# Optimization experiments

Hardware: AMD Instinct MI355X
Metric: run time of the kernel (lower is better)

The kernel has to match this reference:

```python
import jax, jax.numpy as jnp
import numpy as np

LOCAL_SIZE = 128
LN_EPS = 1e-5


def _ln(x):
    # F.layer_norm over last axis, no affine params
    mu = jnp.mean(x, axis=-1, keepdims=True)
    var = jnp.var(x, axis=-1, keepdims=True)
    return (x - mu) / jnp.sqrt(var + LN_EPS)


def _rel_shift(x):
    # x: [b, n, qlen, klen] -> Transformer-XL relative shift
    b, n, q, k = x.shape
    xp = jnp.pad(x, ((0, 0), (0, 0), (0, 0), (1, 0)))
    xp = xp.reshape(b, n, k + 1, q)
    return xp[:, :, 1:, :].reshape(b, n, q, k)


def setup_inputs() -> dict:
    key = jax.random.key(0)
    ks = jax.random.split(key, 12)
    bsz, d_model, qlen, mlen = 16, 1024, 256, 256
    n_head, d_head, d_inner = 16, 64, 4096
    klen = qlen + mlen
    s = 0.02  # param init scale
    return {
        "z1ss": jax.random.normal(ks[0], (bsz, d_model, qlen), jnp.float32),
        "uss": jax.random.normal(ks[1], (bsz, 3 * n_head * d_head, klen), jnp.float32) * 0.1,
        "mems": jax.random.normal(ks[2], (bsz, d_model, mlen), jnp.float32),
        "pos_emb": jax.random.normal(ks[3], (d_model, klen), jnp.float32),
        "Wqkv": jax.random.normal(ks[4], (3 * n_head * d_head, d_model), jnp.float32) * s,
        "Wr": jax.random.normal(ks[5], (n_head * d_head, d_model), jnp.float32) * s,
        "Wo": jax.random.normal(ks[6], (d_model, n_head * d_head), jnp.float32) * s,
        "bo": jnp.zeros((d_model,), jnp.float32),
        "r_w_bias": jax.random.uniform(ks[7], (n_head, d_head), jnp.float32, -0.05, 0.05),
        "r_r_bias": jax.random.uniform(ks[8], (n_head, d_head), jnp.float32, -0.05, 0.05),
        "W1": jax.random.normal(ks[9], (d_inner, d_model), jnp.float32) * s,
        "b1": jnp.zeros((d_inner,), jnp.float32),
        "W2": jax.random.normal(ks[10], (d_model, d_inner), jnp.float32) * s,
        "b2": jnp.zeros((d_model,), jnp.float32),
    }


def reference(z1ss, uss, mems, pos_emb, Wqkv, Wr, Wo, bo, r_w_bias, r_r_bias, W1, b1, W2, b2):
    bsz, d_model, qlen = z1ss.shape
    mlen = mems.shape[-1]
    n_head, d_head = r_w_bias.shape
    scale = 1.0 / (d_head ** 0.5)

    # ---- self-attention with relative positions ----
    cat = jnp.concatenate([mems, z1ss], axis=-1)            # [b, d, klen]
    klen = cat.shape[-1]
    w_heads = jnp.einsum('od,bdk->bok', Wqkv, cat) + uss     # [b, 3*n*dh, klen]
    r_head_k = (Wr @ pos_emb).reshape(n_head, d_head, -1)    # [n, dh, rlen]

    q, k, v = jnp.split(w_heads, 3, axis=1)
    q = q[:, :, -qlen:].reshape(bsz, n_head, d_head, qlen)   # [b, n, dh, q]
    k = k.reshape(bsz, n_head, d_head, klen)
    v = v.reshape(bsz, n_head, d_head, klen)

    AC = jnp.einsum('bndi,bndj->bnij', q + r_w_bias[:, :, None], k)
    BD = jnp.einsum('bndi,ndj->bnij', q + r_r_bias[:, :, None], r_head_k)
    BD = _rel_shift(BD)
    attn_score = (AC + BD) * scale                            # [b, n, q, klen]

    # causal + local-window mask
    i = jnp.arange(qlen)[:, None]
    j = jnp.arange(klen)[None, :]
    mask = (j > i + mlen) | (j <= i + mlen - LOCAL_SIZE)      # [q, klen]
    attn_score = jnp.where(mask[None, None], -1e30, attn_score)

    attn_prob = jax.nn.softmax(attn_score, axis=-1)
    attn_vec = jnp.einsum('bnij,bndj->bndi', attn_prob, v)    # [b, n, dh, q]
    attn_vec = attn_vec.reshape(bsz, n_head * d_head, qlen)
    attn_out = jnp.einsum('od,bdq->boq', Wo, attn_vec) + bo[None, :, None]

    # post-LN residual (pre_lnorm=False), work in [b, q, d]
    h = _ln((attn_out + z1ss).transpose(0, 2, 1))             # [b, q, d]

    # ---- position-wise FF ----
    ff = jax.nn.relu(jnp.einsum('bqd,id->bqi', h, W1) + b1)
    ff = jnp.einsum('bqi,di->bqd', ff, W2) + b2
    out = _ln(ff + h)                                          # [b, q, d]
    return out.transpose(0, 2, 1)                              # [b, d, q]
```

## Files before the change

kernel.cpp:

```cpp
#include <hip/hip_runtime.h>
#include <hip/hip_bf16.h>
#include <math.h>

#define BSZ    16
#define DMODEL 1024
#define QLEN   256
#define MLEN   256
#define KLEN   512
#define NHEAD  16
#define DHEAD  64
#define DINNER 4096

typedef __bf16 bf16;
typedef bf16 bf16x8 __attribute__((ext_vector_type(8)));
typedef float f32x4 __attribute__((ext_vector_type(4)));

#define GLOBAL_AS __attribute__((address_space(1)))
#define LDS_AS    __attribute__((address_space(3)))

__global__ __launch_bounds__(256) void prep_k(
    const float* __restrict__ Wqkv, const float* __restrict__ Wr,
    const float* __restrict__ Wo,   const float* __restrict__ W1,
    const float* __restrict__ W2,   const float* __restrict__ uss,
    const float* __restrict__ mems, const float* __restrict__ z1ss,
    const float* __restrict__ pos_emb,
    bf16* __restrict__ WqkvB, bf16* __restrict__ WrB, bf16* __restrict__ WoB,
    bf16* __restrict__ W1B,   bf16* __restrict__ W2B, bf16* __restrict__ ussV,
    bf16* __restrict__ catT,  bf16* __restrict__ posT,
    bf16* __restrict__ ussQ,  bf16* __restrict__ ussK)
{
    if (blockIdx.x < 21504) {
        long long i = (long long)blockIdx.x * 256 + threadIdx.x;
        const float* src; bf16* dst; long long soff, doff;
        if      (i <  786432) { src = Wqkv; dst = WqkvB; soff = doff = i; }
        else if (i < 1048576) { src = Wr;   dst = WrB;   soff = doff = i -  786432; }
        else if (i < 1310720) { src = Wo;   dst = WoB;   soff = doff = i - 1048576; }
        else if (i < 2359296) { src = W1;   dst = W1B;   soff = doff = i - 1310720; }
        else if (i < 3407872) { src = W2;   dst = W2B;   soff = doff = i - 2359296; }
        else {
            long long u = i - 3407872, b = u >> 17, r = u & 131071;
            src = uss; dst = ussV; soff = b * 393216 + 262144 + r; doff = u;
        }
        float4 v = ((const float4*)src)[soff];
        bf16 b0 = (bf16)v.x, b1 = (bf16)v.y, b2 = (bf16)v.z, b3 = (bf16)v.w;
        union { ushort u[4]; uint2 d; } p;
        p.u[0] = *(ushort*)&b0; p.u[1] = *(ushort*)&b1;
        p.u[2] = *(ushort*)&b2; p.u[3] = *(ushort*)&b3;
        ((uint2*)dst)[doff] = p.d;
        return;
    }
    __shared__ float tile[32][33];
    int blk = blockIdx.x - 21504;
    const float* src; bf16* dst; long long soff, dof; int ld, ldo, tr, tc;
    if (blk < 8192) {
        int bh = blk >> 8, t = blk & 255;
        int b = bh >> 1, half = bh & 1;
        tr = t >> 3; tc = t & 7;
        src = half ? z1ss : mems; soff = (long long)b * 1024 * 256; ld = 256;
        dst = catT; dof = ((long long)b * 512 + half * 256) * 1024; ldo = 1024;
    } else if (blk < 8704) {
        int u = blk - 8192; tr = u >> 4; tc = u & 15;
        src = pos_emb; soff = 0; ld = 512;
        dst = posT; dof = 0; ldo = 1024;
    } else if (blk < 12800) {
        int u = blk - 8704; int b = u >> 8, t = u & 255;
        tr = t >> 3; tc = t & 7;
        src = uss; soff = (long long)b * 3072 * 512 + 256; ld = 512;
        dst = ussQ; dof = (long long)b * 256 * 1024; ldo = 1024;
    } else {
        int u = blk - 12800; int b = u >> 9, t = u & 511;
        tr = t >> 4; tc = t & 15;
        src = uss; soff = ((long long)b * 3072 + 1024) * 512; ld = 512;
        dst = ussK; dof = (long long)b * 512 * 1024; ldo = 1024;
    }
    int tx = threadIdx.x & 31, ty = threadIdx.x >> 5;
    const float* ip = src + soff;
#pragma unroll
    for (int yy = ty; yy < 32; yy += 8)
        tile[yy][tx] = ip[(long long)(tr * 32 + yy) * ld + tc * 32 + tx];
    __syncthreads();
#pragma unroll
    for (int yy = ty; yy < 32; yy += 8)
        dst[dof + (long long)(tc * 32 + yy) * ldo + tr * 32 + tx] = (bf16)tile[tx][yy];
}

__global__ __launch_bounds__(256) void qkv_gemm_k(
    const bf16* __restrict__ catT, const bf16* __restrict__ WqkvB,
    const bf16* __restrict__ posT, const bf16* __restrict__ WrB,
    const bf16* __restrict__ ussQ, const bf16* __restrict__ ussK,
    const bf16* __restrict__ ussV,
    bf16* __restrict__ qT, bf16* __restrict__ kT,
    bf16* __restrict__ rhkT, bf16* __restrict__ vB)
{
    __shared__ bf16 lA[2 * 128 * 32];
    __shared__ bf16 lB[2 * 128 * 32];

    int f = blockIdx.x;
    int id = (f & 7) * 164 + (f >> 3);
    int t = threadIdx.x;
    int w = t >> 6, lane = t & 63;

    const bf16 *Ap, *Bp;
    int mode, bz = 0, m0, n0;
    if (id < 768) {
        bz = id / 48; int r = id % 48;
        if (r < 32) { m0 = 256 + ((r >> 4) << 7); n0 = (r & 15) << 7; }
        else        { int rr = r - 32; m0 = (rr >> 3) << 7; n0 = (8 + (rr & 7)) << 7; }
        Ap = catT + (long long)bz * 512 * 1024; Bp = WqkvB; mode = 0;
    } else if (id < 800) {
        int rr = id - 768; m0 = (rr >> 3) << 7; n0 = (rr & 7) << 7;
        Ap = posT; Bp = WrB; mode = 1;
    } else {
        int rr = id - 800; bz = rr >> 5; int tt = rr & 31;
        m0 = (tt >> 2) << 7; n0 = (tt & 3) << 7;
        Ap = WqkvB + 2048 * 1024; Bp = catT + (long long)bz * 512 * 1024; mode = 2;
    }

    int q = lane >> 4, r16 = lane & 15;
    int wm = w >> 1, wn = w & 1;

    f32x4 acc[4][4];
#pragma unroll
    for (int i = 0; i < 4; ++i)
#pragma unroll
        for (int j = 0; j < 4; ++j)
            acc[i][j] = (f32x4){0.f, 0.f, 0.f, 0.f};

    int srow = lane >> 2;
    int scol = (lane & 3) * 8;

    for (int k0 = 0; k0 < 1024; k0 += 64) {
        __syncthreads();
#pragma unroll
        for (int half = 0; half < 2; ++half) {
#pragma unroll
            for (int issue = 0; issue < 2; ++issue) {
                int c = issue * 4 + w;
                int row = c * 16 + srow;
                int col = k0 + half * 32 + scol;
                __builtin_amdgcn_global_load_lds(
                    (const GLOBAL_AS void*)(Ap + (long long)(m0 + row) * 1024 + col),
                    (LDS_AS void*)(lA + half * 4096 + c * 512 + lane * 8), 16, 0, 0);
                __builtin_amdgcn_global_load_lds(
                    (const GLOBAL_AS void*)(Bp + (long long)(n0 + row) * 1024 + col),
                    (LDS_AS void*)(lB + half * 4096 + c * 512 + lane * 8), 16, 0, 0);
            }
        }
        __syncthreads();
#pragma unroll
        for (int kh = 0; kh < 2; ++kh) {
            bf16x8 af[4], bfr[4];
#pragma unroll
            for (int i = 0; i < 4; ++i)
                af[i] = *(const bf16x8*)&lA[kh * 4096 + (wm * 64 + i * 16 + r16) * 32 + q * 8];
#pragma unroll
            for (int j = 0; j < 4; ++j)
                bfr[j] = *(const bf16x8*)&lB[kh * 4096 + (wn * 64 + j * 16 + r16) * 32 + q * 8];
#pragma unroll
            for (int i = 0; i < 4; ++i)
#pragma unroll
                for (int j = 0; j < 4; ++j)
                    acc[i][j] = __builtin_amdgcn_mfma_f32_16x16x32_bf16(
                        af[i], bfr[j], acc[i][j], 0, 0, 0);
        }
    }

    bool isq = (mode == 0) && (n0 < 1024);
#pragma unroll
    for (int i = 0; i < 4; ++i) {
#pragma unroll
        for (int r = 0; r < 4; ++r) {
            int m = m0 + wm * 64 + i * 16 + q * 4 + r;
#pragma unroll
            for (int j = 0; j < 4; ++j) {
                int n = n0 + wn * 64 + j * 16 + r16;
                float v = acc[i][j][r];
                if (mode == 1) {
                    rhkT[(long long)m * 1024 + n] = (bf16)v;
                } else if (mode == 2) {
                    long long idx = ((long long)bz * 1024 + m) * 512 + n;
                    vB[idx] = (bf16)(v + (float)ussV[idx]);
                } else if (isq) {
                    long long idx = ((long long)(bz * 256 + m - 256) << 10) + n;
                    qT[idx] = (bf16)(v + (float)ussQ[idx]);
                } else {
                    long long idx = ((long long)(bz * 512 + m) << 10) + (n - 1024);
                    kT[idx] = (bf16)(v + (float)ussK[idx]);
                }
            }
        }
    }
}


__device__ __forceinline__ void stage_a_unit(const bf16* __restrict__ Ag, int ldK,
                                             bf16* sAbuf, int qa, int t) {
    int r  = (t >> 2) & 63;
    int ks = t >> 8;
    int cc = (t & 3) ^ (((t >> 5) & 1) << 1);
    int col = ks * 32 + cc * 8;
    __builtin_amdgcn_global_load_lds(
        (const GLOBAL_AS void*)(Ag + (long long)(qa * 64 + r) * ldK + col),
        (LDS_AS void*)(sAbuf + qa * 4096 + t * 8), 16, 0, 0);
    __builtin_amdgcn_global_load_lds(
        (const GLOBAL_AS void*)(Ag + (long long)(qa * 64 + 128 + r) * ldK + col),
        (LDS_AS void*)(sAbuf + (qa + 2) * 4096 + t * 8), 16, 0, 0);
}

__device__ __forceinline__ void stage_b_unit(const bf16* __restrict__ Bg, int ldK,
                                             bf16* sBbuf, int qb, int t) {
#pragma unroll
    for (int j = 0; j < 2; ++j) {
        int u  = j * 512 + t;
        int p  = u >> 8;
        int w8 = u & 255;
        int ks = w8 >> 7;
        int r  = (w8 >> 2) & 31;
        int cc = (u & 3) ^ (((t >> 5) & 1) << 1);
        __builtin_amdgcn_global_load_lds(
            (const GLOBAL_AS void*)(Bg + (long long)(p * 64 + qb * 32 + r) * ldK + ks * 32 + cc * 8),
            (LDS_AS void*)(sBbuf + p * 4096 + ks * 2048 + qb * 1024 + r * 32 + (u & 3) * 8),
            16, 0, 0);
    }
}

__device__ __forceinline__ void ld_a(const bf16* sAbuf, int qa, int wm, int lane,
                                     bf16x8 a[4][2]) {
    int r16 = lane & 15, qq = lane >> 4;
    int flip = ((r16 >> 3) & 1) << 4;
    const bf16* base = sAbuf + (wm * 2 + qa) * 4096;
#pragma unroll
    for (int mf = 0; mf < 4; ++mf)
#pragma unroll
        for (int ks = 0; ks < 2; ++ks)
            a[mf][ks] = *(const bf16x8*)(base +
                ((ks * 2048 + (mf * 16 + r16) * 32 + qq * 8) ^ flip));
}

__device__ __forceinline__ void ld_b(const bf16* sBbuf, int qb, int wn, int lane,
                                     bf16x8 b[2][2]) {
    int r16 = lane & 15, qq = lane >> 4;
    int flip = ((r16 >> 3) & 1) << 4;
    const bf16* base = sBbuf + wn * 4096 + qb * 1024;
#pragma unroll
    for (int nf = 0; nf < 2; ++nf)
#pragma unroll
        for (int ks = 0; ks < 2; ++ks)
            b[nf][ks] = *(const bf16x8*)(base +
                ((ks * 2048 + (nf * 16 + r16) * 32 + qq * 8) ^ flip));
}

#define PH_SYNC_MFMA(QA, QB)                                                   \
    __builtin_amdgcn_s_barrier();                                              \
    asm volatile("s_waitcnt lgkmcnt(0)" ::: "memory");                         \
    __builtin_amdgcn_s_setprio(1);                                             \
    _Pragma("unroll") for (int ks = 0; ks < 2; ++ks)                           \
    _Pragma("unroll") for (int mf = 0; mf < 4; ++mf)                           \
    _Pragma("unroll") for (int nf = 0; nf < 2; ++nf)                           \
        acc[(QA)*4+mf][(QB)*2+nf] = __builtin_amdgcn_mfma_f32_16x16x32_bf16(   \
            a[mf][ks], b[nf][ks], acc[(QA)*4+mf][(QB)*2+nf], 0, 0, 0);         \
    __builtin_amdgcn_s_setprio(0);                                             \
    __builtin_amdgcn_s_barrier();

__device__ __forceinline__ void gemm8_core(
    const bf16* __restrict__ Ap, const bf16* __restrict__ Bp,
    int ldK, int NT, bf16* sA, bf16* sB, f32x4 (&acc)[8][4])
{
    int t = threadIdx.x;
    int lane = t & 63, w = t >> 6;
    int wm = w >> 2, wn = w & 3;

    stage_a_unit(Ap, ldK, sA, 0, t);
    stage_a_unit(Ap, ldK, sA, 1, t);
    stage_b_unit(Bp, ldK, sB, 0, t);
    stage_b_unit(Bp, ldK, sB, 1, t);
    stage_b_unit(Bp + 64, ldK, sB + 16384, 0, t);
    stage_a_unit(Ap + 64, ldK, sA + 16384, 1, t);
    stage_b_unit(Bp + 64, ldK, sB + 16384, 1, t);
    asm volatile("s_waitcnt vmcnt(6)" ::: "memory");
    __builtin_amdgcn_s_barrier();

    bf16x8 a[4][2], b[2][2];
    for (int g = 0; g < NT; ++g) {
        bf16* AR = sA + (g & 1) * 16384;
        bf16* BR = sB + (g & 1) * 16384;
        bf16* AO = sA + ((g & 1) ^ 1) * 16384;
        const bf16* An = Ap + (long long)(g + 1) * 64;
        const bf16* A2 = Ap + (long long)(g + 2) * 64;
        const bf16* B2 = Bp + (long long)(g + 2) * 64;
        ld_a(AR, 0, wm, lane, a);
        ld_b(BR, 0, wn, lane, b);
        if (g + 1 < NT) stage_a_unit(An, ldK, AO, 0, t);
        PH_SYNC_MFMA(0, 0)
        ld_a(AR, 1, wm, lane, a);
        if (g + 2 < NT) stage_b_unit(B2, ldK, BR, 0, t);
        PH_SYNC_MFMA(1, 0)
        ld_b(BR, 1, wn, lane, b);
        if (g + 2 < NT) stage_a_unit(A2, ldK, AR, 1, t);
        PH_SYNC_MFMA(1, 1)
        ld_a(AR, 0, wm, lane, a);
        if (g + 2 < NT) stage_b_unit(B2, ldK, BR, 1, t);
        if (g < NT - 2) asm volatile("s_waitcnt vmcnt(6)" ::: "memory");
        else            asm volatile("s_waitcnt vmcnt(0)" ::: "memory");
        PH_SYNC_MFMA(0, 1)
    }
}

__global__ __launch_bounds__(512) void gemm8_k(
    const bf16* __restrict__ A, const bf16* __restrict__ B,
    int N, int K, int kChunk,
    const float* __restrict__ bias, int relu,
    bf16* __restrict__ outB,
    float* __restrict__ outF1, float* __restrict__ outF2)
{
    __shared__ bf16 sm[65536];
    int nwg = gridDim.x, f = blockIdx.x;
    int xcd = f & 7, l = f >> 3;
    int q8 = nwg >> 3, rm = nwg & 7;
    int wg = (xcd < rm) ? (xcd * (q8 + 1) + l)
                        : (rm * (q8 + 1) + (xcd - rm) * q8 + l);
    int ntn = N >> 8;

    int Keff = K, split = 0, tile = wg;
    const bf16* Ap = A;
    const bf16* Bp = B;
    if (kChunk > 0) {
        int nsplit = K / kChunk;
        int tiles = nwg / nsplit;
        split = wg / tiles; tile = wg % tiles;
        Ap += (long long)split * kChunk;
        Bp += (long long)split * kChunk;
        Keff = kChunk;
    }
    int m0 = (tile / ntn) << 8, n0 = (tile % ntn) << 8;

    f32x4 acc[8][4];
#pragma unroll
    for (int i = 0; i < 8; ++i)
#pragma unroll
        for (int j = 0; j < 4; ++j) acc[i][j] = (f32x4){0.f, 0.f, 0.f, 0.f};

    gemm8_core(Ap + (long long)m0 * K, Bp + (long long)n0 * K, K, Keff >> 6,
               sm, sm + 32768, acc);

    int t = threadIdx.x, lane = t & 63, w = t >> 6;
    int wm = w >> 2, wn = w & 3;
    int qq = lane >> 4, r16 = lane & 15;
    if (outB) {
#pragma unroll
        for (int mf = 0; mf < 8; ++mf) {
#pragma unroll
            for (int rr2 = 0; rr2 < 4; ++rr2) {
                int m = m0 + wm * 128 + mf * 16 + qq * 4 + rr2;
#pragma unroll
                for (int nf = 0; nf < 4; ++nf) {
                    int n = n0 + wn * 64 + nf * 16 + r16;
                    float v = acc[mf][nf][rr2];
                    if (bias) v += bias[n];
                    if (relu) v = fmaxf(v, 0.f);
                    outB[(long long)m * N + n] = (bf16)v;
                }
            }
        }
    } else {
        float* oF = ((split & 2) ? outF2 : outF1) + (long long)(split & 1) * 4194304;
#pragma unroll
        for (int mf = 0; mf < 8; ++mf) {
#pragma unroll
            for (int rr2 = 0; rr2 < 4; ++rr2) {
                int m = m0 + wm * 128 + mf * 16 + qq * 4 + rr2;
#pragma unroll
                for (int nf = 0; nf < 4; ++nf) {
                    int n = n0 + wn * 64 + nf * 16 + r16;
                    oF[(long long)m * N + n] = acc[mf][nf][rr2];
                }
            }
        }
    }
}

__global__ __launch_bounds__(256) void gemm_bf16(
    const bf16* __restrict__ A, const bf16* __restrict__ B,
    int M, int N, int K, int kChunk,
    const float* __restrict__ bias, int relu,
    float* __restrict__ outF, long long ofBatch,
    bf16* __restrict__ outB)
{
    __shared__ bf16 lA[2 * 128 * 32];
    __shared__ bf16 lB[2 * 128 * 32];

    int t = threadIdx.x;
    int w = t >> 6, lane = t & 63;
    int m0 = blockIdx.y * 128, n0 = blockIdx.x * 128;
    int bz = blockIdx.z;

    const bf16* Ap = A;
    const bf16* Bp = B;
    float* oF = outF;
    int Keff = K;
    if (kChunk > 0) {
        Ap = A + (long long)bz * kChunk;
        Bp = B + (long long)bz * kChunk;
        if (outF) oF = outF + (long long)bz * ofBatch;
        Keff = kChunk;
    }

    int q = lane >> 4, r16 = lane & 15;
    int wm = w >> 1, wn = w & 1;

    f32x4 acc[4][4];
#pragma unroll
    for (int i = 0; i < 4; ++i)
#pragma unroll
        for (int j = 0; j < 4; ++j)
            acc[i][j] = (f32x4){0.f, 0.f, 0.f, 0.f};

    int srow = lane >> 2;
    int scol = (lane & 3) * 8;

    for (int k0 = 0; k0 < Keff; k0 += 64) {
        __syncthreads();
#pragma unroll
        for (int half = 0; half < 2; ++half) {
#pragma unroll
            for (int issue = 0; issue < 2; ++issue) {
                int c = issue * 4 + w;
                int row = c * 16 + srow;
                int col = k0 + half * 32 + scol;
                __builtin_amdgcn_global_load_lds(
                    (const GLOBAL_AS void*)(Ap + (long long)(m0 + row) * K + col),
                    (LDS_AS void*)(lA + half * 4096 + c * 512 + lane * 8), 16, 0, 0);
                __builtin_amdgcn_global_load_lds(
                    (const GLOBAL_AS void*)(Bp + (long long)(n0 + row) * K + col),
                    (LDS_AS void*)(lB + half * 4096 + c * 512 + lane * 8), 16, 0, 0);
            }
        }
        __syncthreads();
#pragma unroll
        for (int kh = 0; kh < 2; ++kh) {
            bf16x8 af[4], bfr[4];
#pragma unroll
            for (int i = 0; i < 4; ++i)
                af[i] = *(const bf16x8*)&lA[kh * 4096 + (wm * 64 + i * 16 + r16) * 32 + q * 8];
#pragma unroll
            for (int j = 0; j < 4; ++j)
                bfr[j] = *(const bf16x8*)&lB[kh * 4096 + (wn * 64 + j * 16 + r16) * 32 + q * 8];
#pragma unroll
            for (int i = 0; i < 4; ++i)
#pragma unroll
                for (int j = 0; j < 4; ++j)
                    acc[i][j] = __builtin_amdgcn_mfma_f32_16x16x32_bf16(
                        af[i], bfr[j], acc[i][j], 0, 0, 0);
        }
    }

#pragma unroll
    for (int i = 0; i < 4; ++i) {
#pragma unroll
        for (int r = 0; r < 4; ++r) {
            int m = m0 + wm * 64 + i * 16 + q * 4 + r;
#pragma unroll
            for (int j = 0; j < 4; ++j) {
                int n = n0 + wn * 64 + j * 16 + r16;
                float v = acc[i][j][r];
                if (bias) v += bias[n];
                if (relu) v = fmaxf(v, 0.f);
                if (oF)   oF[(long long)m * N + n] = v;
                if (outB) outB[(long long)m * N + n] = (bf16)v;
            }
        }
    }
}

__global__ __launch_bounds__(256) void attn_mfma_k(
    const bf16* __restrict__ qT,
    const bf16* __restrict__ kT,
    const bf16* __restrict__ vB,
    const bf16* __restrict__ rhkT,
    const float* __restrict__ rwb,
    const float* __restrict__ rrb,
    bf16* __restrict__ avT)
{
    __shared__ float sBD[64][132];

    int t = threadIdx.x;
    int w = t >> 6, lane = t & 63;
    int lo = lane & 15, hi = lane >> 4;
    int i0 = blockIdx.x * 64;
    int n  = blockIdx.y;
    int b  = blockIdx.z;

    const bf16* qp = qT + ((long long)(b * 256 + i0 + 16 * w + lo)) * 1024 + n * 64;
    bf16x8 qw[2], qr[2];
#pragma unroll
    for (int ks = 0; ks < 2; ++ks) {
        bf16x8 qv = *(const bf16x8*)(qp + ks * 32 + hi * 8);
        const float* wb = rwb + n * 64 + ks * 32 + hi * 8;
        const float* rb = rrb + n * 64 + ks * 32 + hi * 8;
#pragma unroll
        for (int e = 0; e < 8; ++e) {
            float qf = (float)qv[e];
            qw[ks][e] = (bf16)(qf + wb[e]);
            qr[ks][e] = (bf16)(qf + rb[e]);
        }
    }

    const bf16* rp = rhkT + (long long)384 * 1024 + n * 64;
#pragma unroll
    for (int tj = 0; tj < 8; ++tj) {
        const bf16* bp = rp + (long long)(16 * tj + lo) * 1024;
        f32x4 a = (f32x4){0.f, 0.f, 0.f, 0.f};
        a = __builtin_amdgcn_mfma_f32_16x16x32_bf16(qr[0], *(const bf16x8*)(bp + hi * 8), a, 0, 0, 0);
        a = __builtin_amdgcn_mfma_f32_16x16x32_bf16(qr[1], *(const bf16x8*)(bp + 32 + hi * 8), a, 0, 0, 0);
#pragma unroll
        for (int r = 0; r < 4; ++r)
            sBD[16 * w + hi * 4 + r][16 * tj + lo] = a[r];
    }
    __syncthreads();

    f32x4 ac[12];
    const bf16* kp = kT + ((long long)b * 512 + i0 + 129) * 1024 + n * 64;
#pragma unroll
    for (int tj = 0; tj < 12; ++tj) {
        const bf16* bp = kp + (long long)(16 * tj + lo) * 1024;
        f32x4 a = (f32x4){0.f, 0.f, 0.f, 0.f};
        a = __builtin_amdgcn_mfma_f32_16x16x32_bf16(qw[0], *(const bf16x8*)(bp + hi * 8), a, 0, 0, 0);
        a = __builtin_amdgcn_mfma_f32_16x16x32_bf16(qw[1], *(const bf16x8*)(bp + 32 + hi * 8), a, 0, 0, 0);
        ac[tj] = a;
    }

    float p[12][4], rowmax[4], rowsum[4];
#pragma unroll
    for (int r = 0; r < 4; ++r) rowmax[r] = -1e30f;
#pragma unroll
    for (int tj = 0; tj < 12; ++tj) {
#pragma unroll
        for (int r = 0; r < 4; ++r) {
            int m = 16 * w + hi * 4 + r;
            int jj = 16 * tj + lo;
            int tt = jj - m;
            float v = (tt >= 0 && tt < 128) ? (ac[tj][r] + sBD[m][tt]) * 0.125f
                                            : -1e30f;
            p[tj][r] = v;
            rowmax[r] = fmaxf(rowmax[r], v);
        }
    }
#pragma unroll
    for (int r = 0; r < 4; ++r) {
        float mx = rowmax[r];
#pragma unroll
        for (int msk = 1; msk < 16; msk <<= 1)
            mx = fmaxf(mx, __shfl_xor(mx, msk, 64));
        rowmax[r] = mx;
        rowsum[r] = 0.f;
    }
#pragma unroll
    for (int tj = 0; tj < 12; ++tj) {
#pragma unroll
        for (int r = 0; r < 4; ++r) {
            float e = exp2f((p[tj][r] - rowmax[r]) * 1.44269504f);
            p[tj][r] = e;
            rowsum[r] += e;
        }
    }
#pragma unroll
    for (int r = 0; r < 4; ++r) {
        float s = rowsum[r];
#pragma unroll
        for (int msk = 1; msk < 16; msk <<= 1)
            s += __shfl_xor(s, msk, 64);
        rowsum[r] = 1.f / s;
    }

    bf16* P = (bf16*)&sBD[0][0];
#pragma unroll
    for (int tj = 0; tj < 12; ++tj) {
#pragma unroll
        for (int r = 0; r < 4; ++r) {
            int m = 16 * w + hi * 4 + r;
            P[m * 264 + 16 * tj + lo] = (bf16)(p[tj][r] * rowsum[r]);
        }
    }
    __syncthreads();

    f32x4 oacc[4];
#pragma unroll
    for (int td = 0; td < 4; ++td) oacc[td] = (f32x4){0.f, 0.f, 0.f, 0.f};
    const bf16* vp = vB + ((long long)b * 1024 + n * 64) * 512 + i0 + 129;
#pragma unroll
    for (int ks = 0; ks < 6; ++ks) {
        bf16x8 af = *(const bf16x8*)(P + (16 * w + lo) * 264 + ks * 32 + hi * 8);
#pragma unroll
        for (int td = 0; td < 4; ++td) {
            bf16x8 bv = *(const bf16x8*)(vp + (long long)(16 * td + lo) * 512 + ks * 32 + hi * 8);
            oacc[td] = __builtin_amdgcn_mfma_f32_16x16x32_bf16(af, bv, oacc[td], 0, 0, 0);
        }
    }
    bf16* op = avT + ((long long)(b * 256 + i0 + 16 * w)) * 1024 + n * 64;
#pragma unroll
    for (int td = 0; td < 4; ++td)
#pragma unroll
        for (int r = 0; r < 4; ++r)
            op[(long long)(hi * 4 + r) * 1024 + 16 * td + lo] = (bf16)oacc[td][r];
}

__global__ __launch_bounds__(256) void ln_bf16_k(
    const float* __restrict__ X1a, const float* __restrict__ X1b,
    const float* __restrict__ bo,  const bf16* __restrict__ catT,
    bf16* __restrict__ H)
{
    int row = blockIdx.x, t = threadIdx.x;
    __shared__ float r1[256], r2[256];
    const float* xa = X1a + (long long)row * 1024;
    const float* xb = X1b + (long long)row * 1024;
    const bf16*  zr = catT + ((long long)(row >> 8) * 512 + 256 + (row & 255)) * 1024;
    float v[4], s = 0.f, ss = 0.f;
#pragma unroll
    for (int u = 0; u < 4; ++u) {
        int c = t + u * 256;
        v[u] = xa[c] + xb[c] + bo[c] + (float)zr[c];
        s += v[u]; ss += v[u] * v[u];
    }
    r1[t] = s; r2[t] = ss;
    __syncthreads();
    for (int off = 128; off > 0; off >>= 1) {
        if (t < off) { r1[t] += r1[t + off]; r2[t] += r2[t + off]; }
        __syncthreads();
    }
    float mean = r1[0] * (1.f / 1024.f);
    float var  = r2[0] * (1.f / 1024.f) - mean * mean;
    float rstd = rsqrtf(var + 1e-5f);
    bf16* hr = H + (long long)row * 1024;
#pragma unroll
    for (int u = 0; u < 4; ++u)
        hr[t + u * 256] = (bf16)((v[u] - mean) * rstd);
}

__global__ __launch_bounds__(256) void ln_final_k(
    const bf16* __restrict__ Hb,
    const float* __restrict__ X2a, const float* __restrict__ X2b,
    const float* __restrict__ X2c, const float* __restrict__ X2d,
    const float* __restrict__ b2,
    float* __restrict__ O)
{
    int row = blockIdx.x, t = threadIdx.x;
    int b = row >> 8, qq = row & 255;
    __shared__ float r1[256], r2[256];
    const float* xa = X2a + (long long)row * 1024;
    const float* xb = X2b + (long long)row * 1024;
    const float* xc = X2c + (long long)row * 1024;
    const float* xd = X2d + (long long)row * 1024;
    const bf16*  hr = Hb  + (long long)row * 1024;

    float y[4], s = 0.f, ss = 0.f;
#pragma unroll
    for (int u = 0; u < 4; ++u) {
        int c = t + u * 256;
        y[u] = xa[c] + xb[c] + xc[c] + xd[c] + b2[c] + (float)hr[c];
        s += y[u]; ss += y[u] * y[u];
    }
    r1[t] = s; r2[t] = ss;
    __syncthreads();
    for (int off = 128; off > 0; off >>= 1) {
        if (t < off) { r1[t] += r1[t + off]; r2[t] += r2[t + off]; }
        __syncthreads();
    }
    float mean = r1[0] * (1.f / 1024.f);
    float var  = r2[0] * (1.f / 1024.f) - mean * mean;
    float rstd = rsqrtf(var + 1e-5f);

    float* ob = O + (long long)b * 1024 * 256 + qq;
#pragma unroll
    for (int u = 0; u < 4; ++u)
        ob[(long long)(t + u * 256) * 256] = (y[u] - mean) * rstd;
}

extern "C" void kernel_launch(void* const* d_in, const int* in_sizes, int n_in,
                              void* d_out, int out_size, void* d_ws, size_t ws_size,
                              hipStream_t stream) {
    const float* z1ss    = (const float*)d_in[0];
    const float* uss     = (const float*)d_in[1];
    const float* mems    = (const float*)d_in[2];
    const float* pos_emb = (const float*)d_in[3];
    const float* Wqkv    = (const float*)d_in[4];
    const float* Wr      = (const float*)d_in[5];
    const float* Wo      = (const float*)d_in[6];
    const float* bo      = (const float*)d_in[7];
    const float* rwb     = (const float*)d_in[8];
    const float* rrb     = (const float*)d_in[9];
    const float* W1      = (const float*)d_in[10];
    const float* b1      = (const float*)d_in[11];
    const float* W2      = (const float*)d_in[12];
    const float* b2      = (const float*)d_in[13];

    char* base = (char*)d_ws;
    bf16*  catT  = (bf16*) (base + 0);
    bf16*  posT  = (bf16*) (base + 16777216);
    bf16*  WqkvB = (bf16*) (base + 17825792);
    bf16*  WrB   = (bf16*) (base + 24117248);
    bf16*  WoB   = (bf16*) (base + 26214400);
    bf16*  W1B   = (bf16*) (base + 28311552);
    bf16*  W2B   = (bf16*) (base + 36700160);
    bf16*  qTB   = (bf16*) (base + 45088768);
    bf16*  kTB   = (bf16*) (base + 53477376);
    bf16*  vBB   = (bf16*) (base + 70254592);
    float* x1a   = (float*)(base + 53477376);
    float* x1b   = (float*)(base + 70254592);
    bf16*  ff_b  = (bf16*) (base + 53477376);
    bf16*  rhkTB = (bf16*) (base + 87031808);
    bf16*  avTB  = (bf16*) (base + 88080384);
    bf16*  ussQb = (bf16*) (base + 96468992);
    bf16*  ussKb = (bf16*) (base + 104857600);
    bf16*  ussVb = (bf16*) (base + 121634816);
    float* x2a   = (float*)(base + 96468992);
    float* x2b   = (float*)(base + 113246208);
    float* x2c   = (float*)(base + 0);
    float* x2d   = (float*)(base + 16777216);
    bf16*  hB    = (bf16*) (base + 130023424);

    prep_k<<<42496, 256, 0, stream>>>(
        Wqkv, Wr, Wo, W1, W2, uss, mems, z1ss, pos_emb,
        WqkvB, WrB, WoB, W1B, W2B, ussVb, catT, posT, ussQb, ussKb);

    qkv_gemm_k<<<1312, 256, 0, stream>>>(
        catT, WqkvB, posT, WrB, ussQb, ussKb, ussVb, qTB, kTB, rhkTB, vBB);

    attn_mfma_k<<<dim3(4, NHEAD, BSZ), 256, 0, stream>>>(
        qTB, kTB, vBB, rhkTB, rwb, rrb, avTB);

    gemm_bf16<<<dim3(8, 32, 2), 256, 0, stream>>>(
        avTB, WoB, 4096, 1024, 1024, 512,
        nullptr, 0, x1a, (long long)(x1b - x1a), nullptr);

    ln_bf16_k<<<4096, 256, 0, stream>>>(x1a, x1b, bo, catT, hB);

    gemm8_k<<<256, 512, 0, stream>>>(
        hB, W1B, 4096, 1024, 0, b1, 1, ff_b, nullptr, nullptr);

    gemm8_k<<<256, 512, 0, stream>>>(
        ff_b, W2B, 1024, 4096, 1024, nullptr, 0, nullptr,
        x2c , x2a );

    ln_final_k<<<4096, 256, 0, stream>>>(
        hB, x2c, x2d, x2a, x2b, b2, (float*)d_out);
}
```

Before: 578.6 us.

## Route output projection through gemm8 with 4-way split-K and drop gemm_bf16

Replaces the generic 128x128-tile gemm_bf16 used for the Wo projection with the larger-tile 512-thread gemm8_k kernel in a 4-way split-K mode. The layer-norm kernel is widened to sum four partial outputs instead of two. This removes the old kernel and is meant to get better MFMA utilisation and data reuse per block. In exchange the LN step reads more fp32 partials. The QKV GEMM's block-index swizzle is also removed, which changes the block scheduling order.

Result: no change. 575.9 us (-0.5%).

```diff
diff --git a/kernel.cpp b/kernel.cpp
--- a/kernel.cpp
+++ b/kernel.cpp
@@ -95,8 +95,7 @@
     __shared__ bf16 lA[2 * 128 * 32];
     __shared__ bf16 lB[2 * 128 * 32];
 
-    int f = blockIdx.x;
-    int id = (f & 7) * 164 + (f >> 3);
+    int id = blockIdx.x;
     int t = threadIdx.x;
     int w = t >> 6, lane = t & 63;
 
@@ -379,99 +378,6 @@
     }
 }
 
-__global__ __launch_bounds__(256) void gemm_bf16(
-    const bf16* __restrict__ A, const bf16* __restrict__ B,
-    int M, int N, int K, int kChunk,
-    const float* __restrict__ bias, int relu,
-    float* __restrict__ outF, long long ofBatch,
-    bf16* __restrict__ outB)
-{
-    __shared__ bf16 lA[2 * 128 * 32];
-    __shared__ bf16 lB[2 * 128 * 32];
-
-    int t = threadIdx.x;
-    int w = t >> 6, lane = t & 63;
-    int m0 = blockIdx.y * 128, n0 = blockIdx.x * 128;
-    int bz = blockIdx.z;
-
-    const bf16* Ap = A;
-    const bf16* Bp = B;
-    float* oF = outF;
-    int Keff = K;
-    if (kChunk > 0) {
-        Ap = A + (long long)bz * kChunk;
-        Bp = B + (long long)bz * kChunk;
-        if (outF) oF = outF + (long long)bz * ofBatch;
-        Keff = kChunk;
-    }
-
-    int q = lane >> 4, r16 = lane & 15;
-    int wm = w >> 1, wn = w & 1;
-
-    f32x4 acc[4][4];
-#pragma unroll
-    for (int i = 0; i < 4; ++i)
-#pragma unroll
-        for (int j = 0; j < 4; ++j)
-            acc[i][j] = (f32x4){0.f, 0.f, 0.f, 0.f};
-
-    int srow = lane >> 2;
-    int scol = (lane & 3) * 8;
-
-    for (int k0 = 0; k0 < Keff; k0 += 64) {
-        __syncthreads();
-#pragma unroll
-        for (int half = 0; half < 2; ++half) {
-#pragma unroll
-            for (int issue = 0; issue < 2; ++issue) {
-                int c = issue * 4 + w;
-                int row = c * 16 + srow;
-                int col = k0 + half * 32 + scol;
-                __builtin_amdgcn_global_load_lds(
-                    (const GLOBAL_AS void*)(Ap + (long long)(m0 + row) * K + col),
-                    (LDS_AS void*)(lA + half * 4096 + c * 512 + lane * 8), 16, 0, 0);
-                __builtin_amdgcn_global_load_lds(
-                    (const GLOBAL_AS void*)(Bp + (long long)(n0 + row) * K + col),
-                    (LDS_AS void*)(lB + half * 4096 + c * 512 + lane * 8), 16, 0, 0);
-            }
-        }
-        __syncthreads();
-#pragma unroll
-        for (int kh = 0; kh < 2; ++kh) {
-            bf16x8 af[4], bfr[4];
-#pragma unroll
-            for (int i = 0; i < 4; ++i)
-                af[i] = *(const bf16x8*)&lA[kh * 4096 + (wm * 64 + i * 16 + r16) * 32 + q * 8];
-#pragma unroll
-            for (int j = 0; j < 4; ++j)
-                bfr[j] = *(const bf16x8*)&lB[kh * 4096 + (wn * 64 + j * 16 + r16) * 32 + q * 8];
-#pragma unroll
-            for (int i = 0; i < 4; ++i)
-#pragma unroll
-                for (int j = 0; j < 4; ++j)
-                    acc[i][j] = __builtin_amdgcn_mfma_f32_16x16x32_bf16(
-                        af[i], bfr[j], acc[i][j], 0, 0, 0);
-        }
-    }
-
-#pragma unroll
-    for (int i = 0; i < 4; ++i) {
-#pragma unroll
-        for (int r = 0; r < 4; ++r) {
-            int m = m0 + wm * 64 + i * 16 + q * 4 + r;
-#pragma unroll
-            for (int j = 0; j < 4; ++j) {
-                int n = n0 + wn * 64 + j * 16 + r16;
-                float v = acc[i][j][r];
-                if (bias) v += bias[n];
-                if (relu) v = fmaxf(v, 0.f);
-                if (oF)   oF[(long long)m * N + n] = v;
-                if (outB) outB[(long long)m * N + n] = (bf16)v;
-            }
-        }
-    }
-}
-
 __global__ __launch_bounds__(256) void attn_mfma_k(
     const bf16* __restrict__ qT,
     const bf16* __restrict__ kT,
@@ -606,6 +512,7 @@
 
 __global__ __launch_bounds__(256) void ln_bf16_k(
     const float* __restrict__ X1a, const float* __restrict__ X1b,
+    const float* __restrict__ X1c, const float* __restrict__ X1d,
     const float* __restrict__ bo,  const bf16* __restrict__ catT,
     bf16* __restrict__ H)
 {
@@ -613,12 +520,14 @@
     __shared__ float r1[256], r2[256];
     const float* xa = X1a + (long long)row * 1024;
     const float* xb = X1b + (long long)row * 1024;
+    const float* xc = X1c + (long long)row * 1024;
+    const float* xd = X1d + (long long)row * 1024;
     const bf16*  zr = catT + ((long long)(row >> 8) * 512 + 256 + (row & 255)) * 1024;
     float v[4], s = 0.f, ss = 0.f;
 #pragma unroll
     for (int u = 0; u < 4; ++u) {
         int c = t + u * 256;
-        v[u] = xa[c] + xb[c] + bo[c] + (float)zr[c];
+        v[u] = xa[c] + xb[c] + xc[c] + xd[c] + bo[c] + (float)zr[c];
         s += v[u]; ss += v[u] * v[u];
     }
     r1[t] = s; r2[t] = ss;
@@ -706,6 +615,8 @@
     bf16*  vBB   = (bf16*) (base + 70254592);
     float* x1a   = (float*)(base + 53477376);
     float* x1b   = (float*)(base + 70254592);
+    float* x1c   = (float*)(base + 96468992);
+    float* x1d   = (float*)(base + 113246208);
     bf16*  ff_b  = (bf16*) (base + 53477376);
     bf16*  rhkTB = (bf16*) (base + 87031808);
     bf16*  avTB  = (bf16*) (base + 88080384);
@@ -728,11 +639,11 @@
     attn_mfma_k<<<dim3(4, NHEAD, BSZ), 256, 0, stream>>>(
         qTB, kTB, vBB, rhkTB, rwb, rrb, avTB);
 
-    gemm_bf16<<<dim3(8, 32, 2), 256, 0, stream>>>(
-        avTB, WoB, 4096, 1024, 1024, 512,
-        nullptr, 0, x1a, (long long)(x1b - x1a), nullptr);
-
-    ln_bf16_k<<<4096, 256, 0, stream>>>(x1a, x1b, bo, catT, hB);
+    gemm8_k<<<256, 512, 0, stream>>>(
+        avTB, WoB, 1024, 1024, 256, nullptr, 0, nullptr,
+        x1a , x1c );
+
+    ln_bf16_k<<<4096, 256, 0, stream>>>(x1a, x1b, x1c, x1d, bo, catT, hB);
 
     gemm8_k<<<256, 512, 0, stream>>>(
         hB, W1B, 4096, 1024, 0, b1, 1, ff_b, nullptr, nullptr);
```
